# Kernel tuning notes

Measured on AMD Instinct MI355X. Metric: run time of the kernel, lower is better.

The kernel has to match this reference:

```python
import jax, jax.numpy as jnp
import numpy as np


def gcn_conv(h, edge_index, num_nodes):
    # Symmetric-normalized GCN aggregation: out[i] = sum_{(j->i)} h[j] / sqrt(deg(i)*deg(j))
    row, col = edge_index[0], edge_index[1]
    deg = jax.ops.segment_sum(jnp.ones(col.shape, dtype=h.dtype), col, num_segments=num_nodes)
    d_inv_sqrt = jnp.where(deg > 0, jax.lax.rsqrt(jnp.maximum(deg, 1.0)), 0.0)
    w = d_inv_sqrt[row] * d_inv_sqrt[col]           # [E]
    msg = h[row] * w[:, None]                        # [E, D] gather + scale
    return jax.ops.segment_sum(msg, col, num_segments=num_nodes)  # [N, D] scatter-add


def setup_inputs() -> dict:
    key = jax.random.key(0)
    k1, k2, k3, k4 = jax.random.split(key, 4)
    N, E, F_IN, F_HID, F_OUT = 100000, 1600000, 128, 64, 40
    x = jax.random.normal(k1, (N, F_IN), dtype=jnp.float32)
    edge_index = jax.random.randint(k2, (2, E), 0, N, dtype=jnp.int64)
    # xavier_uniform with gain=1.414 (as in reset_parameters); biases zero
    def xavier(k, shape, gain=1.414):
        fan_out, fan_in = shape
        a = gain * np.sqrt(6.0 / (fan_in + fan_out))
        return jax.random.uniform(k, shape, jnp.float32, -a, a)
    W1 = xavier(k3, (F_HID, F_IN))
    b1 = jnp.zeros((F_HID,), dtype=jnp.float32)
    W2 = xavier(k4, (F_OUT, F_HID))
    b2 = jnp.zeros((F_OUT,), dtype=jnp.float32)
    return {"x": x, "edge_index": edge_index, "W1": W1, "b1": b1, "W2": W2, "b2": b2}


def reference(x, edge_index, W1, b1, W2, b2):
    # GNN.forward with num_layers=2, use_mp=True, eval mode (dropout inactive)
    N = x.shape[0]
    h = x @ W1.T                      # [N, nhid]
    h = gcn_conv(h, edge_index, N)
    h = jax.nn.relu(h + b1)
    h = h @ W2.T                      # [N, nclass]
    h = gcn_conv(h, edge_index, N)
    return h + b2
```

## Files before the change

kernel.cpp:

```cpp
#include <hip/hip_runtime.h>
#include <hip/hip_fp16.h>


typedef __attribute__((ext_vector_type(8))) _Float16 half8v;
typedef __attribute__((ext_vector_type(4))) float   float4v;

__global__ void k_binfill(const int* __restrict__ ed,
                          int* __restrict__ gbincnt, unsigned* __restrict__ binbuf,
                          int E, int cap) {
  __shared__ int hist[512];
  __shared__ int cursor[512];
  __shared__ unsigned rec[4096];
  __shared__ unsigned short binv[4096];
  __shared__ int s_is64;
  int t = threadIdx.x;
  hist[t] = 0; hist[t + 256] = 0;
  if (t == 0) s_is64 = 1;
  __syncthreads();
  {
    int any = 0;
    #pragma unroll
    for (int u = 0; u < 8; ++u) {
      int idx = 2 * (t * 8 + u) + 1;
      if (idx < 2 * E && ed[idx] != 0) any = 1;
    }
    if (any) s_is64 = 0;
  }
  __syncthreads();
  const int is64 = s_is64;
  const int base = blockIdx.x * 4096;
  const int nE = min(4096, E - base);
  for (int j = t; j < nE; j += 256) {
    int e = base + j;
    int r = is64 ? ed[2 * e] : ed[e];
    int c = is64 ? ed[2 * (E + e)] : ed[E + e];
    rec[j] = (unsigned)r | ((unsigned)(c & 255) << 17);
    binv[j] = (unsigned short)(c >> 8);
    atomicAdd(&hist[c >> 8], 1);
  }
  __syncthreads();
  for (int b = t; b < 512; b += 256) {
    int h = hist[b];
    cursor[b] = h ? atomicAdd(&gbincnt[b], h) : 0;
  }
  __syncthreads();
  for (int j = t; j < nE; j += 256) {
    int bin = binv[j];
    int pos = atomicAdd(&cursor[bin], 1);
    if (pos < cap)
      binbuf[(size_t)bin * cap + pos] = rec[j];
  }
}

__global__ void k_degscat(const unsigned* __restrict__ binbuf, const int* __restrict__ gbincnt,
                          float* __restrict__ dis, int* __restrict__ rowptr,
                          int* __restrict__ srcs, int NBINS, int N, int cap) {
  __shared__ int sd[512];
  __shared__ int cnt[256];
  __shared__ int sc[256];
  __shared__ int cursor[256];
  __shared__ unsigned rec[8192];
  int t = threadIdx.x, b = blockIdx.x;
  sd[t]       = (t < NBINS)       ? min(gbincnt[t], cap)       : 0;
  sd[t + 256] = (t + 256 < NBINS) ? min(gbincnt[t + 256], cap) : 0;
  cnt[t] = 0;
  __syncthreads();
  for (int off = 1; off < 512; off <<= 1) {
    int v0 = (t >= off) ? sd[t - off] : 0;
    int v1 = sd[t + 256 - off];
    __syncthreads();
    sd[t] += v0; sd[t + 256] += v1;
    __syncthreads();
  }
  const int mybase = (b == 0) ? 0 : sd[b - 1];
  if (b == NBINS - 1 && t == 0) rowptr[N] = sd[NBINS - 1];

  int n = min(gbincnt[b], cap);
  const unsigned* buf = binbuf + (size_t)b * cap;
  for (int j = t; j < n; j += 256) {
    unsigned v = buf[j];
    rec[j] = v;
    atomicAdd(&cnt[v >> 17], 1);
  }
  __syncthreads();
  sc[t] = cnt[t];
  __syncthreads();
  for (int off = 1; off < 256; off <<= 1) {
    int v = (t >= off) ? sc[t - off] : 0;
    __syncthreads();
    sc[t] += v;
    __syncthreads();
  }
  int rp = mybase + ((t == 0) ? 0 : sc[t - 1]);
  cursor[t] = rp;
  int node = b * 256 + t;
  if (node < N) {
    int d = cnt[t];
    dis[node] = (d > 0) ? rsqrtf((float)d) : 0.f;
    rowptr[node] = rp;
  }
  __syncthreads();
  for (int j = t; j < n; j += 256) {
    unsigned v = rec[j];
    int pos = atomicAdd(&cursor[v >> 17], 1);
    srcs[pos] = (int)(v & 0x1FFFF);
  }
}

__launch_bounds__(256)
__global__ void k_gemm1_mfma(const float* __restrict__ X, const float* __restrict__ W,
                             const float* __restrict__ dis, unsigned char* __restrict__ h1q,
                             float* __restrict__ sc1, int N) {
  __shared__ _Float16 wl[64 * 128];
  const int t = threadIdx.x;
  const int row0 = blockIdx.x * 128;
  const int w = t >> 6, l = t & 63;
  const int m0 = w * 32;
  const int lr = l & 15, q = l >> 4;

  float4 xr[4][2][2];
  #pragma unroll
  for (int kc = 0; kc < 4; ++kc) {
    #pragma unroll
    for (int mt = 0; mt < 2; ++mt) {
      int row = min(row0 + m0 + mt * 16 + lr, N - 1);
      const float* p = &X[(size_t)row * 128 + kc * 32 + q * 8];
      xr[kc][mt][0] = *(const float4*)p;
      xr[kc][mt][1] = *(const float4*)(p + 4);
    }
  }

  #pragma unroll
  for (int j = 0; j < 8; ++j) {
    int qq = t + 256 * j;
    int r = qq >> 5, k4 = qq & 31;
    float4 v = *(const float4*)&W[(size_t)r * 128 + k4 * 4];
    _Float16 h4[4] = {(_Float16)v.x, (_Float16)v.y, (_Float16)v.z, (_Float16)v.w};
    int k = (k4 * 4) ^ ((r & 7) * 8);
    *(float2*)&wl[r * 128 + k] = *(float2*)h4;
  }
  __syncthreads();

  float4v acc[2][4] = {};
  #pragma unroll
  for (int kc = 0; kc < 4; ++kc) {
    half8v a[2], b[4];
    #pragma unroll
    for (int mt = 0; mt < 2; ++mt) {
      float4 v0 = xr[kc][mt][0], v1 = xr[kc][mt][1];
      _Float16 h8[8] = {(_Float16)v0.x, (_Float16)v0.y, (_Float16)v0.z, (_Float16)v0.w,
                        (_Float16)v1.x, (_Float16)v1.y, (_Float16)v1.z, (_Float16)v1.w};
      a[mt] = *(half8v*)h8;
    }
    #pragma unroll
    for (int nt = 0; nt < 4; ++nt) {
      int n = nt * 16 + lr;
      int k = (kc * 32 + q * 8) ^ ((n & 7) * 8);
      b[nt] = *(half8v*)&wl[n * 128 + k];
    }
    #pragma unroll
    for (int mt = 0; mt < 2; ++mt)
      #pragma unroll
      for (int nt = 0; nt < 4; ++nt)
        acc[mt][nt] = __builtin_amdgcn_mfma_f32_16x16x32_f16(a[mt], b[nt], acc[mt][nt], 0, 0, 0);
  }

  #pragma unroll
  for (int mt = 0; mt < 2; ++mt) {
    #pragma unroll
    for (int r = 0; r < 4; ++r) {
      int row = row0 + m0 + mt * 16 + q * 4 + r;
      if (row < N) {
        float dr = dis[row];
        float v0 = acc[mt][0][r] * dr;
        float v1 = acc[mt][1][r] * dr;
        float v2 = acc[mt][2][r] * dr;
        float v3 = acc[mt][3][r] * dr;
        float m = fmaxf(fmaxf(fabsf(v0), fabsf(v1)), fmaxf(fabsf(v2), fabsf(v3)));
        #pragma unroll
        for (int off = 1; off < 16; off <<= 1)
          m = fmaxf(m, __shfl_xor(m, off));
        float inv = (m > 0.f) ? (127.f / m) : 0.f;
        unsigned char* dst = h1q + (size_t)row * 64;
        int q0 = (int)rintf(v0 * inv);
        int q1 = (int)rintf(v1 * inv);
        int q2 = (int)rintf(v2 * inv);
        int q3 = (int)rintf(v3 * inv);
        q0 = max(-127, min(127, q0));
        q1 = max(-127, min(127, q1));
        q2 = max(-127, min(127, q2));
        q3 = max(-127, min(127, q3));
        dst[lr]      = (unsigned char)(signed char)q0;
        dst[lr + 16] = (unsigned char)(signed char)q1;
        dst[lr + 32] = (unsigned char)(signed char)q2;
        dst[lr + 48] = (unsigned char)(signed char)q3;
        if (lr == 0) sc1[row] = m * (1.f / 127.f);
      }
    }
  }
}

__launch_bounds__(256)
__global__ void k_gemm2_mfma(const __half* __restrict__ Xh, const float* __restrict__ W,
                             const float* __restrict__ dis, unsigned char* __restrict__ h2,
                             int N) {
  __shared__ _Float16 xl[128 * 64];
  __shared__ _Float16 wl[48 * 64];
  const int t = threadIdx.x;
  const int row0 = blockIdx.x * 128;

  for (int i = t; i < 48 * 8; i += 256) {
    int c = i >> 3, kq = i & 7;
    _Float16 h8[8];
    #pragma unroll
    for (int j = 0; j < 8; ++j)
      h8[j] = (c < 40) ? (_Float16)W[c * 64 + kq * 8 + j] : (_Float16)0.f;
    *(float4*)&wl[c * 64 + ((kq * 8) ^ ((c & 7) * 8))] = *(float4*)h8;
  }
  for (int i = t; i < 1024; i += 256) {
    int r = i >> 3, kq = i & 7;
    int row = row0 + r;
    float4 v = make_float4(0.f, 0.f, 0.f, 0.f);
    if (row < N) v = *(const float4*)&Xh[(size_t)row * 64 + kq * 8];
    *(float4*)&xl[r * 64 + ((kq * 8) ^ ((r & 7) * 8))] = v;
  }
  __syncthreads();

  const int w = t >> 6, l = t & 63;
  const int m0 = w * 32;
  const int lr = l & 15, q = l >> 4;

  float4v acc[2][3] = {};
  #pragma unroll
  for (int kc = 0; kc < 2; ++kc) {
    half8v a[2], b[3];
    #pragma unroll
    for (int mt = 0; mt < 2; ++mt) {
      int m = m0 + mt * 16 + lr;
      int k = (kc * 32 + q * 8) ^ ((m & 7) * 8);
      a[mt] = *(half8v*)&xl[m * 64 + k];
    }
    #pragma unroll
    for (int nt = 0; nt < 3; ++nt) {
      int n = nt * 16 + lr;
      int k = (kc * 32 + q * 8) ^ ((n & 7) * 8);
      b[nt] = *(half8v*)&wl[n * 64 + k];
    }
    #pragma unroll
    for (int mt = 0; mt < 2; ++mt)
      #pragma unroll
      for (int nt = 0; nt < 3; ++nt)
        acc[mt][nt] = __builtin_amdgcn_mfma_f32_16x16x32_f16(a[mt], b[nt], acc[mt][nt], 0, 0, 0);
  }

  #pragma unroll
  for (int mt = 0; mt < 2; ++mt) {
    #pragma unroll
    for (int r = 0; r < 4; ++r) {
      int row = row0 + m0 + mt * 16 + q * 4 + r;
      if (row < N) {
        float dr = dis[row];
        float v0 = acc[mt][0][r] * dr;
        float v1 = acc[mt][1][r] * dr;
        float v2 = acc[mt][2][r] * dr;
        float m = fmaxf(fabsf(v0), fmaxf(fabsf(v1), fabsf(v2)));
        #pragma unroll
        for (int off = 1; off < 16; off <<= 1)
          m = fmaxf(m, __shfl_xor(m, off));
        float s = m * (1.f / 127.f);
        float inv = (m > 0.f) ? (127.f / m) : 0.f;
        unsigned char* dst = h2 + (size_t)row * 64;
        int q0 = (int)rintf(v0 * inv);
        int q1 = (int)rintf(v1 * inv);
        int q2 = (int)rintf(v2 * inv);
        q0 = max(-127, min(127, q0));
        q1 = max(-127, min(127, q1));
        q2 = max(-127, min(127, q2));
        dst[lr]      = (unsigned char)(signed char)q0;
        dst[lr + 16] = (unsigned char)(signed char)q1;
        if (lr + 32 < 40) dst[lr + 32] = (unsigned char)(signed char)q2;
        if (lr == 0) *(float*)&dst[40] = s;
        if (lr >= 1 && lr <= 5) *(int*)&dst[40 + 4 * lr] = 0;
      }
    }
  }
}

__launch_bounds__(256)
__global__ void k_conv64(const unsigned char* __restrict__ H, const float* __restrict__ sc1,
                         const int* __restrict__ rowptr, const int* __restrict__ srcs,
                         const float* __restrict__ dis, const float* __restrict__ b1,
                         __half* __restrict__ out, int N) {
  int t = threadIdx.x;
  int li = t & 7;
  int node = blockIdx.x * 32 + (t >> 3);
  if (node >= N) return;
  int s = rowptr[node], e = rowptr[node + 1];
  int last = e - 1;
  float a0 = 0.f, a1 = 0.f, a2 = 0.f, a3 = 0.f,
        a4 = 0.f, a5 = 0.f, a6 = 0.f, a7 = 0.f;
  for (int p = s; p < e; p += 4) {
    int s0 = srcs[p];
    int s1 = srcs[min(p + 1, last)];
    int s2 = srcs[min(p + 2, last)];
    int s3 = srcs[min(p + 3, last)];
    uint2 r0 = *(const uint2*)&H[(size_t)s0 * 64 + 8 * li];
    uint2 r1 = *(const uint2*)&H[(size_t)s1 * 64 + 8 * li];
    uint2 r2 = *(const uint2*)&H[(size_t)s2 * 64 + 8 * li];
    uint2 r3 = *(const uint2*)&H[(size_t)s3 * 64 + 8 * li];
    float c0 = sc1[s0], c1 = sc1[s1], c2 = sc1[s2], c3 = sc1[s3];
    {
      int x0 = (int)r0.x, x1 = (int)r0.y;
      a0 = fmaf((float)((x0 << 24) >> 24), c0, a0);
      a1 = fmaf((float)((x0 << 16) >> 24), c0, a1);
      a2 = fmaf((float)((x0 << 8)  >> 24), c0, a2);
      a3 = fmaf((float)( x0        >> 24), c0, a3);
      a4 = fmaf((float)((x1 << 24) >> 24), c0, a4);
      a5 = fmaf((float)((x1 << 16) >> 24), c0, a5);
      a6 = fmaf((float)((x1 << 8)  >> 24), c0, a6);
      a7 = fmaf((float)( x1        >> 24), c0, a7);
    }
    if (p + 1 < e) {
      int x0 = (int)r1.x, x1 = (int)r1.y;
      a0 = fmaf((float)((x0 << 24) >> 24), c1, a0);
      a1 = fmaf((float)((x0 << 16) >> 24), c1, a1);
      a2 = fmaf((float)((x0 << 8)  >> 24), c1, a2);
      a3 = fmaf((float)( x0        >> 24), c1, a3);
      a4 = fmaf((float)((x1 << 24) >> 24), c1, a4);
      a5 = fmaf((float)((x1 << 16) >> 24), c1, a5);
      a6 = fmaf((float)((x1 << 8)  >> 24), c1, a6);
      a7 = fmaf((float)( x1        >> 24), c1, a7);
    }
    if (p + 2 < e) {
      int x0 = (int)r2.x, x1 = (int)r2.y;
      a0 = fmaf((float)((x0 << 24) >> 24), c2, a0);
      a1 = fmaf((float)((x0 << 16) >> 24), c2, a1);
      a2 = fmaf((float)((x0 << 8)  >> 24), c2, a2);
      a3 = fmaf((float)( x0        >> 24), c2, a3);
      a4 = fmaf((float)((x1 << 24) >> 24), c2, a4);
      a5 = fmaf((float)((x1 << 16) >> 24), c2, a5);
      a6 = fmaf((float)((x1 << 8)  >> 24), c2, a6);
      a7 = fmaf((float)( x1        >> 24), c2, a7);
    }
    if (p + 3 < e) {
      int x0 = (int)r3.x, x1 = (int)r3.y;
      a0 = fmaf((float)((x0 << 24) >> 24), c3, a0);
      a1 = fmaf((float)((x0 << 16) >> 24), c3, a1);
      a2 = fmaf((float)((x0 << 8)  >> 24), c3, a2);
      a3 = fmaf((float)( x0        >> 24), c3, a3);
      a4 = fmaf((float)((x1 << 24) >> 24), c3, a4);
      a5 = fmaf((float)((x1 << 16) >> 24), c3, a5);
      a6 = fmaf((float)((x1 << 8)  >> 24), c3, a6);
      a7 = fmaf((float)( x1        >> 24), c3, a7);
    }
  }
  float dn = dis[node];
  const float* bb = b1 + 8 * li;
  __half hv[8];
  hv[0] = __float2half_rn(fmaxf(fmaf(a0, dn, bb[0]), 0.f));
  hv[1] = __float2half_rn(fmaxf(fmaf(a1, dn, bb[1]), 0.f));
  hv[2] = __float2half_rn(fmaxf(fmaf(a2, dn, bb[2]), 0.f));
  hv[3] = __float2half_rn(fmaxf(fmaf(a3, dn, bb[3]), 0.f));
  hv[4] = __float2half_rn(fmaxf(fmaf(a4, dn, bb[4]), 0.f));
  hv[5] = __float2half_rn(fmaxf(fmaf(a5, dn, bb[5]), 0.f));
  hv[6] = __float2half_rn(fmaxf(fmaf(a6, dn, bb[6]), 0.f));
  hv[7] = __float2half_rn(fmaxf(fmaf(a7, dn, bb[7]), 0.f));
  *(float4*)&out[(size_t)node * 64 + 8 * li] = *(float4*)hv;
}

__launch_bounds__(256)
__global__ void k_conv40(const unsigned char* __restrict__ H, const int* __restrict__ rowptr,
                         const int* __restrict__ srcs, const float* __restrict__ dis,
                         const float* __restrict__ b2, float* __restrict__ out, int N) {
  int t = threadIdx.x;
  int li = t & 7;
  int node = blockIdx.x * 32 + (t >> 3);
  if (node >= N) return;
  bool act = li < 5;
  int s = rowptr[node], e = rowptr[node + 1];
  int last = e - 1;
  float a0 = 0.f, a1 = 0.f, a2 = 0.f, a3 = 0.f,
        a4 = 0.f, a5 = 0.f, a6 = 0.f, a7 = 0.f;
  for (int p = s; p < e; p += 4) {
    int s0 = srcs[p];
    int s1 = srcs[min(p + 1, last)];
    int s2 = srcs[min(p + 2, last)];
    int s3 = srcs[min(p + 3, last)];
    if (act) {
      const unsigned char* p0 = &H[(size_t)s0 * 64];
      const unsigned char* p1 = &H[(size_t)s1 * 64];
      const unsigned char* p2 = &H[(size_t)s2 * 64];
      const unsigned char* p3 = &H[(size_t)s3 * 64];
      uint2 r0 = *(const uint2*)&p0[8 * li];
      uint2 r1 = *(const uint2*)&p1[8 * li];
      uint2 r2 = *(const uint2*)&p2[8 * li];
      uint2 r3 = *(const uint2*)&p3[8 * li];
      float c0 = *(const float*)&p0[40];
      float c1 = *(const float*)&p1[40];
      float c2 = *(const float*)&p2[40];
      float c3 = *(const float*)&p3[40];
      {
        int x0 = (int)r0.x, x1 = (int)r0.y;
        a0 = fmaf((float)((x0 << 24) >> 24), c0, a0);
        a1 = fmaf((float)((x0 << 16) >> 24), c0, a1);
        a2 = fmaf((float)((x0 << 8)  >> 24), c0, a2);
        a3 = fmaf((float)( x0        >> 24), c0, a3);
        a4 = fmaf((float)((x1 << 24) >> 24), c0, a4);
        a5 = fmaf((float)((x1 << 16) >> 24), c0, a5);
        a6 = fmaf((float)((x1 << 8)  >> 24), c0, a6);
        a7 = fmaf((float)( x1        >> 24), c0, a7);
      }
      if (p + 1 < e) {
        int x0 = (int)r1.x, x1 = (int)r1.y;
        a0 = fmaf((float)((x0 << 24) >> 24), c1, a0);
        a1 = fmaf((float)((x0 << 16) >> 24), c1, a1);
        a2 = fmaf((float)((x0 << 8)  >> 24), c1, a2);
        a3 = fmaf((float)( x0        >> 24), c1, a3);
        a4 = fmaf((float)((x1 << 24) >> 24), c1, a4);
        a5 = fmaf((float)((x1 << 16) >> 24), c1, a5);
        a6 = fmaf((float)((x1 << 8)  >> 24), c1, a6);
        a7 = fmaf((float)( x1        >> 24), c1, a7);
      }
      if (p + 2 < e) {
        int x0 = (int)r2.x, x1 = (int)r2.y;
        a0 = fmaf((float)((x0 << 24) >> 24), c2, a0);
        a1 = fmaf((float)((x0 << 16) >> 24), c2, a1);
        a2 = fmaf((float)((x0 << 8)  >> 24), c2, a2);
        a3 = fmaf((float)( x0        >> 24), c2, a3);
        a4 = fmaf((float)((x1 << 24) >> 24), c2, a4);
        a5 = fmaf((float)((x1 << 16) >> 24), c2, a5);
        a6 = fmaf((float)((x1 << 8)  >> 24), c2, a6);
        a7 = fmaf((float)( x1        >> 24), c2, a7);
      }
      if (p + 3 < e) {
        int x0 = (int)r3.x, x1 = (int)r3.y;
        a0 = fmaf((float)((x0 << 24) >> 24), c3, a0);
        a1 = fmaf((float)((x0 << 16) >> 24), c3, a1);
        a2 = fmaf((float)((x0 << 8)  >> 24), c3, a2);
        a3 = fmaf((float)( x0        >> 24), c3, a3);
        a4 = fmaf((float)((x1 << 24) >> 24), c3, a4);
        a5 = fmaf((float)((x1 << 16) >> 24), c3, a5);
        a6 = fmaf((float)((x1 << 8)  >> 24), c3, a6);
        a7 = fmaf((float)( x1        >> 24), c3, a7);
      }
    }
  }
  if (act) {
    float dn = dis[node];
    const float* bb = b2 + 8 * li;
    float4 v0 = make_float4(fmaf(a0, dn, bb[0]), fmaf(a1, dn, bb[1]),
                            fmaf(a2, dn, bb[2]), fmaf(a3, dn, bb[3]));
    float4 v1 = make_float4(fmaf(a4, dn, bb[4]), fmaf(a5, dn, bb[5]),
                            fmaf(a6, dn, bb[6]), fmaf(a7, dn, bb[7]));
    *(float4*)&out[(size_t)node * 40 + 8 * li] = v0;
    *(float4*)&out[(size_t)node * 40 + 8 * li + 4] = v1;
  }
}

extern "C" void kernel_launch(void* const* d_in, const int* in_sizes, int n_in,
                              void* d_out, int out_size, void* d_ws, size_t ws_size,
                              hipStream_t stream) {
  const float* x  = (const float*)d_in[0];
  const int*   ed = (const int*)d_in[1];
  const float* W1 = (const float*)d_in[2];
  const float* b1 = (const float*)d_in[3];
  const float* W2 = (const float*)d_in[4];
  const float* b2 = (const float*)d_in[5];
  float* out = (float*)d_out;

  const int FIN = 128, FH = 64;
  const int N = in_sizes[0] / FIN;
  const int E = in_sizes[1] / 2;
  const int NBINS = (N + 255) >> 8;

  char* ws = (char*)d_ws;
  size_t off = 0;
  auto alloc = [&](size_t bytes) {
    void* p = ws + off;
    off = (off + bytes + 255) & ~(size_t)255;
    return p;
  };
  int*           gbincnt = (int*)alloc(512 * 4);
  float*         dis     = (float*)alloc((size_t)N * 4);
  int*           rowptr  = (int*)alloc(((size_t)N + 1) * 4);
  int*           srcs    = (int*)alloc((size_t)E * 4);
  unsigned char* h1q     = (unsigned char*)alloc((size_t)N * FH * 2);
  __half*        h1b     = (__half*)alloc((size_t)N * FH * 2);
  unsigned char* h2      = (unsigned char*)alloc((size_t)N * 64);
  float* sc1 = (float*)(h1q + (((size_t)N * 64 + 255) & ~(size_t)255));
  int cap = (int)(((size_t)N * FH * 2) / ((size_t)NBINS * 4));
  if (cap > 8192) cap = 8192;
  unsigned* binbuf = (unsigned*)h1q;

  hipMemsetAsync(gbincnt, 0, 512 * 4, stream);

  int fb = (E + 4095) / 4096;
  k_binfill<<<fb, 256, 0, stream>>>(ed, gbincnt, binbuf, E, cap);
  k_degscat<<<NBINS, 256, 0, stream>>>(binbuf, gbincnt, dis, rowptr, srcs, NBINS, N, cap);

  int mb = (N + 127) / 128;
  int cb = (N + 31) / 32;
  k_gemm1_mfma<<<mb, 256, 0, stream>>>(x, W1, dis, h1q, sc1, N);
  k_conv64<<<cb, 256, 0, stream>>>(h1q, sc1, rowptr, srcs, dis, b1, h1b, N);
  k_gemm2_mfma<<<mb, 256, 0, stream>>>(h1b, W2, dis, h2, N);
  k_conv40<<<cb, 256, 0, stream>>>(h2, rowptr, srcs, dis, b2, out, N);
}
```

Before: 222.3 us.

## Sort nodes by in-degree within each bin to balance conv warp workloads

k_degscat now counting-sorts the 256 nodes of each bin by in-degree (capped at 254) and writes a per-bin worklist. Both aggregation kernels read node ids from this worklist, so nodes of similar degree share a wavefront and divergent loop trip counts are reduced. The cost is an extra histogram and scan in the degree kernel, an extra indirection per node, and less contiguous output writes and rowptr reads.

New measurement: 235.6 us. 1.06x slower.

```diff
diff --git a/kernel.cpp b/kernel.cpp
--- a/kernel.cpp
+++ b/kernel.cpp
@@ -54,16 +54,20 @@
 
 __global__ void k_degscat(const unsigned* __restrict__ binbuf, const int* __restrict__ gbincnt,
                           float* __restrict__ dis, int* __restrict__ rowptr,
-                          int* __restrict__ srcs, int NBINS, int N, int cap) {
+                          int* __restrict__ srcs, int* __restrict__ worklist,
+                          int NBINS, int N, int cap) {
   __shared__ int sd[512];
   __shared__ int cnt[256];
   __shared__ int sc[256];
   __shared__ int cursor[256];
+  __shared__ int dh[256];
+  __shared__ int dsc[256];
+  __shared__ int dcur[256];
   __shared__ unsigned rec[8192];
   int t = threadIdx.x, b = blockIdx.x;
   sd[t]       = (t < NBINS)       ? min(gbincnt[t], cap)       : 0;
   sd[t + 256] = (t + 256 < NBINS) ? min(gbincnt[t + 256], cap) : 0;
-  cnt[t] = 0;
+  cnt[t] = 0; dh[t] = 0; dcur[t] = 0;
   __syncthreads();
   for (int off = 1; off < 512; off <<= 1) {
     int v0 = (t >= off) ? sd[t - off] : 0;
@@ -94,7 +98,8 @@
   int rp = mybase + ((t == 0) ? 0 : sc[t - 1]);
   cursor[t] = rp;
   int node = b * 256 + t;
-  if (node < N) {
+  bool valid = node < N;
+  if (valid) {
     int d = cnt[t];
     dis[node] = (d > 0) ? rsqrtf((float)d) : 0.f;
     rowptr[node] = rp;
@@ -105,6 +110,21 @@
     int pos = atomicAdd(&cursor[v >> 17], 1);
     srcs[pos] = (int)(v & 0x1FFFF);
   }
+
+  int db = valid ? min(cnt[t], 254) : 255;
+  atomicAdd(&dh[db], 1);
+  __syncthreads();
+  dsc[t] = dh[t];
+  __syncthreads();
+  for (int off = 1; off < 256; off <<= 1) {
+    int v = (t >= off) ? dsc[t - off] : 0;
+    __syncthreads();
+    dsc[t] += v;
+    __syncthreads();
+  }
+  int rbase = (db == 0) ? 0 : dsc[db - 1];
+  int rank = rbase + atomicAdd(&dcur[db], 1);
+  worklist[b * 256 + rank] = valid ? node : 0x7FFFFFFF;
 }
 
 __launch_bounds__(256)
@@ -289,116 +309,27 @@
 __launch_bounds__(256)
 __global__ void k_conv64(const unsigned char* __restrict__ H, const float* __restrict__ sc1,
                          const int* __restrict__ rowptr, const int* __restrict__ srcs,
+                         const int* __restrict__ worklist,
                          const float* __restrict__ dis, const float* __restrict__ b1,
                          __half* __restrict__ out, int N) {
   int t = threadIdx.x;
   int li = t & 7;
-  int node = blockIdx.x * 32 + (t >> 3);
-  if (node >= N) return;
-  int s = rowptr[node], e = rowptr[node + 1];
-  int last = e - 1;
-  float a0 = 0.f, a1 = 0.f, a2 = 0.f, a3 = 0.f,
-        a4 = 0.f, a5 = 0.f, a6 = 0.f, a7 = 0.f;
-  for (int p = s; p < e; p += 4) {
-    int s0 = srcs[p];
-    int s1 = srcs[min(p + 1, last)];
-    int s2 = srcs[min(p + 2, last)];
-    int s3 = srcs[min(p + 3, last)];
-    uint2 r0 = *(const uint2*)&H[(size_t)s0 * 64 + 8 * li];
-    uint2 r1 = *(const uint2*)&H[(size_t)s1 * 64 + 8 * li];
-    uint2 r2 = *(const uint2*)&H[(size_t)s2 * 64 + 8 * li];
-    uint2 r3 = *(const uint2*)&H[(size_t)s3 * 64 + 8 * li];
-    float c0 = sc1[s0], c1 = sc1[s1], c2 = sc1[s2], c3 = sc1[s3];
-    {
-      int x0 = (int)r0.x, x1 = (int)r0.y;
-      a0 = fmaf((float)((x0 << 24) >> 24), c0, a0);
-      a1 = fmaf((float)((x0 << 16) >> 24), c0, a1);
-      a2 = fmaf((float)((x0 << 8)  >> 24), c0, a2);
-      a3 = fmaf((float)( x0        >> 24), c0, a3);
-      a4 = fmaf((float)((x1 << 24) >> 24), c0, a4);
-      a5 = fmaf((float)((x1 << 16) >> 24), c0, a5);
-      a6 = fmaf((float)((x1 << 8)  >> 24), c0, a6);
-      a7 = fmaf((float)( x1        >> 24), c0, a7);
-    }
-    if (p + 1 < e) {
-      int x0 = (int)r1.x, x1 = (int)r1.y;
-      a0 = fmaf((float)((x0 << 24) >> 24), c1, a0);
-      a1 = fmaf((float)((x0 << 16) >> 24), c1, a1);
-      a2 = fmaf((float)((x0 << 8)  >> 24), c1, a2);
-      a3 = fmaf((float)( x0        >> 24), c1, a3);
-      a4 = fmaf((float)((x1 << 24) >> 24), c1, a4);
-      a5 = fmaf((float)((x1 << 16) >> 24), c1, a5);
-      a6 = fmaf((float)((x1 << 8)  >> 24), c1, a6);
-      a7 = fmaf((float)( x1        >> 24), c1, a7);
-    }
-    if (p + 2 < e) {
-      int x0 = (int)r2.x, x1 = (int)r2.y;
-      a0 = fmaf((float)((x0 << 24) >> 24), c2, a0);
-      a1 = fmaf((float)((x0 << 16) >> 24), c2, a1);
-      a2 = fmaf((float)((x0 << 8)  >> 24), c2, a2);
-      a3 = fmaf((float)( x0        >> 24), c2, a3);
-      a4 = fmaf((float)((x1 << 24) >> 24), c2, a4);
-      a5 = fmaf((float)((x1 << 16) >> 24), c2, a5);
-      a6 = fmaf((float)((x1 << 8)  >> 24), c2, a6);
-      a7 = fmaf((float)( x1        >> 24), c2, a7);
-    }
-    if (p + 3 < e) {
-      int x0 = (int)r3.x, x1 = (int)r3.y;
-      a0 = fmaf((float)((x0 << 24) >> 24), c3, a0);
-      a1 = fmaf((float)((x0 << 16) >> 24), c3, a1);
-      a2 = fmaf((float)((x0 << 8)  >> 24), c3, a2);
-      a3 = fmaf((float)( x0        >> 24), c3, a3);
-      a4 = fmaf((float)((x1 << 24) >> 24), c3, a4);
-      a5 = fmaf((float)((x1 << 16) >> 24), c3, a5);
-      a6 = fmaf((float)((x1 << 8)  >> 24), c3, a6);
-      a7 = fmaf((float)( x1        >> 24), c3, a7);
-    }
-  }
-  float dn = dis[node];
-  const float* bb = b1 + 8 * li;
-  __half hv[8];
-  hv[0] = __float2half_rn(fmaxf(fmaf(a0, dn, bb[0]), 0.f));
-  hv[1] = __float2half_rn(fmaxf(fmaf(a1, dn, bb[1]), 0.f));
-  hv[2] = __float2half_rn(fmaxf(fmaf(a2, dn, bb[2]), 0.f));
-  hv[3] = __float2half_rn(fmaxf(fmaf(a3, dn, bb[3]), 0.f));
-  hv[4] = __float2half_rn(fmaxf(fmaf(a4, dn, bb[4]), 0.f));
-  hv[5] = __float2half_rn(fmaxf(fmaf(a5, dn, bb[5]), 0.f));
-  hv[6] = __float2half_rn(fmaxf(fmaf(a6, dn, bb[6]), 0.f));
-  hv[7] = __float2half_rn(fmaxf(fmaf(a7, dn, bb[7]), 0.f));
-  *(float4*)&out[(size_t)node * 64 + 8 * li] = *(float4*)hv;
-}
-
-__launch_bounds__(256)
-__global__ void k_conv40(const unsigned char* __restrict__ H, const int* __restrict__ rowptr,
-                         const int* __restrict__ srcs, const float* __restrict__ dis,
-                         const float* __restrict__ b2, float* __restrict__ out, int N) {
-  int t = threadIdx.x;
-  int li = t & 7;
-  int node = blockIdx.x * 32 + (t >> 3);
-  if (node >= N) return;
-  bool act = li < 5;
-  int s = rowptr[node], e = rowptr[node + 1];
-  int last = e - 1;
-  float a0 = 0.f, a1 = 0.f, a2 = 0.f, a3 = 0.f,
-        a4 = 0.f, a5 = 0.f, a6 = 0.f, a7 = 0.f;
-  for (int p = s; p < e; p += 4) {
-    int s0 = srcs[p];
-    int s1 = srcs[min(p + 1, last)];
-    int s2 = srcs[min(p + 2, last)];
-    int s3 = srcs[min(p + 3, last)];
-    if (act) {
-      const unsigned char* p0 = &H[(size_t)s0 * 64];
-      const unsigned char* p1 = &H[(size_t)s1 * 64];
-      const unsigned char* p2 = &H[(size_t)s2 * 64];
-      const unsigned char* p3 = &H[(size_t)s3 * 64];
-      uint2 r0 = *(const uint2*)&p0[8 * li];
-      uint2 r1 = *(const uint2*)&p1[8 * li];
-      uint2 r2 = *(const uint2*)&p2[8 * li];
-      uint2 r3 = *(const uint2*)&p3[8 * li];
-      float c0 = *(const float*)&p0[40];
-      float c1 = *(const float*)&p1[40];
-      float c2 = *(const float*)&p2[40];
-      float c3 = *(const float*)&p3[40];
+  int node = worklist[blockIdx.x * 32 + (t >> 3)];
+  if (node < N) {
+    int s = rowptr[node], e = rowptr[node + 1];
+    int last = e - 1;
+    float a0 = 0.f, a1 = 0.f, a2 = 0.f, a3 = 0.f,
+          a4 = 0.f, a5 = 0.f, a6 = 0.f, a7 = 0.f;
+    for (int p = s; p < e; p += 4) {
+      int s0 = srcs[p];
+      int s1 = srcs[min(p + 1, last)];
+      int s2 = srcs[min(p + 2, last)];
+      int s3 = srcs[min(p + 3, last)];
+      uint2 r0 = *(const uint2*)&H[(size_t)s0 * 64 + 8 * li];
+      uint2 r1 = *(const uint2*)&H[(size_t)s1 * 64 + 8 * li];
+      uint2 r2 = *(const uint2*)&H[(size_t)s2 * 64 + 8 * li];
+      uint2 r3 = *(const uint2*)&H[(size_t)s3 * 64 + 8 * li];
+      float c0 = sc1[s0], c1 = sc1[s1], c2 = sc1[s2], c3 = sc1[s3];
       {
         int x0 = (int)r0.x, x1 = (int)r0.y;
         a0 = fmaf((float)((x0 << 24) >> 24), c0, a0);
@@ -444,16 +375,109 @@
         a7 = fmaf((float)( x1        >> 24), c3, a7);
       }
     }
-  }
-  if (act) {
     float dn = dis[node];
-    const float* bb = b2 + 8 * li;
-    float4 v0 = make_float4(fmaf(a0, dn, bb[0]), fmaf(a1, dn, bb[1]),
-                            fmaf(a2, dn, bb[2]), fmaf(a3, dn, bb[3]));
-    float4 v1 = make_float4(fmaf(a4, dn, bb[4]), fmaf(a5, dn, bb[5]),
-                            fmaf(a6, dn, bb[6]), fmaf(a7, dn, bb[7]));
-    *(float4*)&out[(size_t)node * 40 + 8 * li] = v0;
-    *(float4*)&out[(size_t)node * 40 + 8 * li + 4] = v1;
+    const float* bb = b1 + 8 * li;
+    __half hv[8];
+    hv[0] = __float2half_rn(fmaxf(fmaf(a0, dn, bb[0]), 0.f));
+    hv[1] = __float2half_rn(fmaxf(fmaf(a1, dn, bb[1]), 0.f));
+    hv[2] = __float2half_rn(fmaxf(fmaf(a2, dn, bb[2]), 0.f));
+    hv[3] = __float2half_rn(fmaxf(fmaf(a3, dn, bb[3]), 0.f));
+    hv[4] = __float2half_rn(fmaxf(fmaf(a4, dn, bb[4]), 0.f));
+    hv[5] = __float2half_rn(fmaxf(fmaf(a5, dn, bb[5]), 0.f));
+    hv[6] = __float2half_rn(fmaxf(fmaf(a6, dn, bb[6]), 0.f));
+    hv[7] = __float2half_rn(fmaxf(fmaf(a7, dn, bb[7]), 0.f));
+    *(float4*)&out[(size_t)node * 64 + 8 * li] = *(float4*)hv;
+  }
+}
+
+__launch_bounds__(256)
+__global__ void k_conv40(const unsigned char* __restrict__ H, const int* __restrict__ rowptr,
+                         const int* __restrict__ srcs, const int* __restrict__ worklist,
+                         const float* __restrict__ dis, const float* __restrict__ b2,
+                         float* __restrict__ out, int N) {
+  int t = threadIdx.x;
+  int li = t & 7;
+  int node = worklist[blockIdx.x * 32 + (t >> 3)];
+  if (node < N) {
+    bool act = li < 5;
+    int s = rowptr[node], e = rowptr[node + 1];
+    int last = e - 1;
+    float a0 = 0.f, a1 = 0.f, a2 = 0.f, a3 = 0.f,
+          a4 = 0.f, a5 = 0.f, a6 = 0.f, a7 = 0.f;
+    for (int p = s; p < e; p += 4) {
+      int s0 = srcs[p];
+      int s1 = srcs[min(p + 1, last)];
+      int s2 = srcs[min(p + 2, last)];
+      int s3 = srcs[min(p + 3, last)];
+      if (act) {
+        const unsigned char* p0 = &H[(size_t)s0 * 64];
+        const unsigned char* p1 = &H[(size_t)s1 * 64];
+        const unsigned char* p2 = &H[(size_t)s2 * 64];
+        const unsigned char* p3 = &H[(size_t)s3 * 64];
+        uint2 r0 = *(const uint2*)&p0[8 * li];
+        uint2 r1 = *(const uint2*)&p1[8 * li];
+        uint2 r2 = *(const uint2*)&p2[8 * li];
+        uint2 r3 = *(const uint2*)&p3[8 * li];
+        float c0 = *(const float*)&p0[40];
+        float c1 = *(const float*)&p1[40];
+        float c2 = *(const float*)&p2[40];
+        float c3 = *(const float*)&p3[40];
+        {
+          int x0 = (int)r0.x, x1 = (int)r0.y;
+          a0 = fmaf((float)((x0 << 24) >> 24), c0, a0);
+          a1 = fmaf((float)((x0 << 16) >> 24), c0, a1);
+          a2 = fmaf((float)((x0 << 8)  >> 24), c0, a2);
+          a3 = fmaf((float)( x0        >> 24), c0, a3);
+          a4 = fmaf((float)((x1 << 24) >> 24), c0, a4);
+          a5 = fmaf((float)((x1 << 16) >> 24), c0, a5);
+          a6 = fmaf((float)((x1 << 8)  >> 24), c0, a6);
+          a7 = fmaf((float)( x1        >> 24), c0, a7);
+        }
+        if (p + 1 < e) {
+          int x0 = (int)r1.x, x1 = (int)r1.y;
+          a0 = fmaf((float)((x0 << 24) >> 24), c1, a0);
+          a1 = fmaf((float)((x0 << 16) >> 24), c1, a1);
+          a2 = fmaf((float)((x0 << 8)  >> 24), c1, a2);
+          a3 = fmaf((float)( x0        >> 24), c1, a3);
+          a4 = fmaf((float)((x1 << 24) >> 24), c1, a4);
+          a5 = fmaf((float)((x1 << 16) >> 24), c1, a5);
+          a6 = fmaf((float)((x1 << 8)  >> 24), c1, a6);
+          a7 = fmaf((float)( x1        >> 24), c1, a7);
+        }
+        if (p + 2 < e) {
+          int x0 = (int)r2.x, x1 = (int)r2.y;
+          a0 = fmaf((float)((x0 << 24) >> 24), c2, a0);
+          a1 = fmaf((float)((x0 << 16) >> 24), c2, a1);
+          a2 = fmaf((float)((x0 << 8)  >> 24), c2, a2);
+          a3 = fmaf((float)( x0        >> 24), c2, a3);
+          a4 = fmaf((float)((x1 << 24) >> 24), c2, a4);
+          a5 = fmaf((float)((x1 << 16) >> 24), c2, a5);
+          a6 = fmaf((float)((x1 << 8)  >> 24), c2, a6);
+          a7 = fmaf((float)( x1        >> 24), c2, a7);
+        }
+        if (p + 3 < e) {
+          int x0 = (int)r3.x, x1 = (int)r3.y;
+          a0 = fmaf((float)((x0 << 24) >> 24), c3, a0);
+          a1 = fmaf((float)((x0 << 16) >> 24), c3, a1);
+          a2 = fmaf((float)((x0 << 8)  >> 24), c3, a2);
+          a3 = fmaf((float)( x0        >> 24), c3, a3);
+          a4 = fmaf((float)((x1 << 24) >> 24), c3, a4);
+          a5 = fmaf((float)((x1 << 16) >> 24), c3, a5);
+          a6 = fmaf((float)((x1 << 8)  >> 24), c3, a6);
+          a7 = fmaf((float)( x1        >> 24), c3, a7);
+        }
+      }
+    }
+    if (act) {
+      float dn = dis[node];
+      const float* bb = b2 + 8 * li;
+      float4 v0 = make_float4(fmaf(a0, dn, bb[0]), fmaf(a1, dn, bb[1]),
+                              fmaf(a2, dn, bb[2]), fmaf(a3, dn, bb[3]));
+      float4 v1 = make_float4(fmaf(a4, dn, bb[4]), fmaf(a5, dn, bb[5]),
+                              fmaf(a6, dn, bb[6]), fmaf(a7, dn, bb[7]));
+      *(float4*)&out[(size_t)node * 40 + 8 * li] = v0;
+      *(float4*)&out[(size_t)node * 40 + 8 * li + 4] = v1;
+    }
   }
 }
 
@@ -480,13 +504,14 @@
     off = (off + bytes + 255) & ~(size_t)255;
     return p;
   };
-  int*           gbincnt = (int*)alloc(512 * 4);
-  float*         dis     = (float*)alloc((size_t)N * 4);
-  int*           rowptr  = (int*)alloc(((size_t)N + 1) * 4);
-  int*           srcs    = (int*)alloc((size_t)E * 4);
-  unsigned char* h1q     = (unsigned char*)alloc((size_t)N * FH * 2);
-  __half*        h1b     = (__half*)alloc((size_t)N * FH * 2);
-  unsigned char* h2      = (unsigned char*)alloc((size_t)N * 64);
+  int*           gbincnt  = (int*)alloc(512 * 4);
+  float*         dis      = (float*)alloc((size_t)N * 4);
+  int*           rowptr   = (int*)alloc(((size_t)N + 1) * 4);
+  int*           srcs     = (int*)alloc((size_t)E * 4);
+  int*           worklist = (int*)alloc((size_t)NBINS * 256 * 4);
+  unsigned char* h1q      = (unsigned char*)alloc((size_t)N * FH * 2);
+  __half*        h1b      = (__half*)alloc((size_t)N * FH * 2);
+  unsigned char* h2       = (unsigned char*)alloc((size_t)N * 64);
   float* sc1 = (float*)(h1q + (((size_t)N * 64 + 255) & ~(size_t)255));
   int cap = (int)(((size_t)N * FH * 2) / ((size_t)NBINS * 4));
   if (cap > 8192) cap = 8192;
@@ -496,12 +521,13 @@
 
   int fb = (E + 4095) / 4096;
   k_binfill<<<fb, 256, 0, stream>>>(ed, gbincnt, binbuf, E, cap);
-  k_degscat<<<NBINS, 256, 0, stream>>>(binbuf, gbincnt, dis, rowptr, srcs, NBINS, N, cap);
+  k_degscat<<<NBINS, 256, 0, stream>>>(binbuf, gbincnt, dis, rowptr, srcs, worklist,
+                                       NBINS, N, cap);
 
   int mb = (N + 127) / 128;
-  int cb = (N + 31) / 32;
+  int cb = NBINS * 8;
   k_gemm1_mfma<<<mb, 256, 0, stream>>>(x, W1, dis, h1q, sc1, N);
-  k_conv64<<<cb, 256, 0, stream>>>(h1q, sc1, rowptr, srcs, dis, b1, h1b, N);
+  k_conv64<<<cb, 256, 0, stream>>>(h1q, sc1, rowptr, srcs, worklist, dis, b1, h1b, N);
   k_gemm2_mfma<<<mb, 256, 0, stream>>>(h1b, W2, dis, h2, N);
-  k_conv40<<<cb, 256, 0, stream>>>(h2, rowptr, srcs, dis, b2, out, N);
-}
+  k_conv40<<<cb, 256, 0, stream>>>(h2, rowptr, srcs, worklist, dis, b2, out, N);
+}
```
